# Performance work log

Hardware: AMD Instinct MI355X
Metric: run time of the kernel (lower is better)

## Reference

```python
import jax, jax.numpy as jnp
import numpy as np

C = 256

def setup_inputs() -> dict:
    key = jax.random.key(0)
    ks = jax.random.split(key, 7)
    s = 1.0 / np.sqrt(C)
    x = jax.random.normal(ks[0], (4, C, 64, 64), dtype=jnp.float32)
    Wq = jax.random.uniform(ks[1], (C, C), jnp.float32, -s, s)
    bq = jax.random.uniform(ks[2], (C,), jnp.float32, -s, s)
    Wk = jax.random.uniform(ks[3], (C, C), jnp.float32, -s, s)
    bk = jax.random.uniform(ks[4], (C,), jnp.float32, -s, s)
    Wv = jax.random.uniform(ks[5], (C, C), jnp.float32, -s, s)
    bv = jax.random.uniform(ks[6], (C,), jnp.float32, -s, s)
    return {"x": x, "Wq": Wq, "bq": bq, "Wk": Wk, "bk": bk, "Wv": Wv, "bv": bv}

def reference(x, Wq, bq, Wk, bk, Wv, bv):
    B, Cc, H, W = x.shape
    N = H * W
    xf = x.reshape(B, Cc, N)                      # (B, C, N)
    # 1x1 conv == channel linear: out[b,o,n] = sum_c W[o,c] x[b,c,n] + b[o]
    q = jnp.einsum('oc,bcn->bno', Wq, xf) + bq    # (B, N, C)  proj_query^T
    k = jnp.einsum('oc,bcn->bon', Wk, xf) + bk[None, :, None]  # (B, C, N)
    v = jnp.einsum('oc,bcn->bon', Wv, xf) + bv[None, :, None]  # (B, C, N)
    energy = jnp.einsum('bnc,bcm->bnm', q, k)     # (B, N, N)
    attention = jax.nn.softmax(energy, axis=-1)
    # out = V @ attention^T : out[b,c,n] = sum_m v[b,c,m] * attention[b,n,m]
    out = jnp.einsum('bcm,bnm->bcn', v, attention)
    return out.reshape(B, Cc, H, W)
```

## Files before the change

kernel.cpp:

```cpp
#include <hip/hip_runtime.h>
#include <math.h>

#define BB 4
#define CC 256
#define NN 4096

using half8 = __attribute__((ext_vector_type(8))) _Float16;
using f32x4 = __attribute__((ext_vector_type(4))) float;

__device__ __forceinline__ unsigned short f2h(float f) {
  _Float16 h = (_Float16)f;
  return __builtin_bit_cast(unsigned short, h);
}

#define ASYNC16(g, l)                                                        \
  __builtin_amdgcn_global_load_lds(                                          \
      (const __attribute__((address_space(1))) unsigned int*)(g),            \
      (__attribute__((address_space(3))) unsigned int*)(l), 16, 0, 0)

__device__ __forceinline__ int kt_off(int r, int chunk) {
  return r * 256 + (((chunk & 24) | ((chunk ^ r) & 7)) << 3);
}
__device__ __forceinline__ int vt_off(int r, int chunk) {
  return r * 64 + (((chunk ^ r) & 7) << 3);
}

__global__ __launch_bounds__(256) void k_transpose(const float* __restrict__ x,
                                                   unsigned short* __restrict__ Xt) {
  __shared__ float tile[64][65];
  int b = blockIdx.z, c0 = blockIdx.y * 64, n0 = blockIdx.x * 64;
  int t = threadIdx.x;
  const float* xp = x + ((size_t)b * CC + c0) * NN + n0;
#pragma unroll
  for (int p = 0; p < 4; ++p) {
    int c = p * 16 + (t >> 4);
    int j = (t & 15) * 4;
    float4 v = *(const float4*)(xp + (size_t)c * NN + j);
    tile[c][j] = v.x; tile[c][j + 1] = v.y; tile[c][j + 2] = v.z; tile[c][j + 3] = v.w;
  }
  __syncthreads();
  unsigned short* xtp = Xt + ((size_t)b * NN + n0) * CC + c0;
#pragma unroll
  for (int p = 0; p < 2; ++p) {
    int n = p * 32 + (t >> 3);
    int cb = (t & 7) * 8;
    union { unsigned short u[8]; uint4 v; } tmp;
#pragma unroll
    for (int i = 0; i < 8; ++i) tmp.u[i] = f2h(tile[cb + i][n]);
    *(uint4*)(xtp + (size_t)n * CC + cb) = tmp.v;
  }
}

__global__ __launch_bounds__(256, 1) void k_proj(const unsigned short* __restrict__ Xt,
    const float* __restrict__ Wq, const float* __restrict__ bq,
    const float* __restrict__ Wk, const float* __restrict__ bk,
    const float* __restrict__ Wv, const float* __restrict__ bv,
    unsigned short* __restrict__ Q, unsigned short* __restrict__ K,
    unsigned short* __restrict__ V) {
  __shared__ union {
    struct { unsigned short xa[128][72]; unsigned short wb[256][72]; } s;
    unsigned short qo[128][264];
    unsigned short vo[256][136];
  } u;
  int proj = blockIdx.z;
  const float* W    = proj == 0 ? Wq : (proj == 1 ? Wk : Wv);
  const float* bias = proj == 0 ? bq : (proj == 1 ? bk : bv);
  int b = blockIdx.y, n0 = blockIdx.x * 128;
  int t = threadIdx.x, w = t >> 6, lane = t & 63, l15 = lane & 15, quad = lane >> 4;

  f32x4 z = {0.f, 0.f, 0.f, 0.f};
  f32x4 acc[2][16];
#pragma unroll
  for (int i = 0; i < 2; ++i)
#pragma unroll
    for (int j = 0; j < 16; ++j) acc[i][j] = z;

  for (int ks = 0; ks < 4; ++ks) {
    __syncthreads();
#pragma unroll
    for (int p = 0; p < 4; ++p) {
      int r = p * 32 + (t >> 3);
      *(uint4*)&u.s.xa[r][(t & 7) * 8] =
        *(const uint4*)(Xt + ((size_t)b * NN + n0 + r) * CC + ks * 64 + (t & 7) * 8);
    }
#pragma unroll
    for (int p = 0; p < 16; ++p) {
      int r = p * 16 + (t >> 4);
      float4 wv = *(const float4*)(W + (size_t)r * CC + ks * 64 + (t & 15) * 4);
      ushort4 pk;
      pk.x = f2h(wv.x); pk.y = f2h(wv.y); pk.z = f2h(wv.z); pk.w = f2h(wv.w);
      *(ushort4*)&u.s.wb[r][(t & 15) * 4] = pk;
    }
    __syncthreads();
#pragma unroll
    for (int kc = 0; kc < 2; ++kc) {
      half8 af[2];
#pragma unroll
      for (int nt = 0; nt < 2; ++nt)
        af[nt] = *(const half8*)&u.s.xa[w * 32 + nt * 16 + l15][kc * 32 + quad * 8];
#pragma unroll
      for (int ct = 0; ct < 16; ++ct) {
        half8 bf = *(const half8*)&u.s.wb[ct * 16 + l15][kc * 32 + quad * 8];
        acc[0][ct] = __builtin_amdgcn_mfma_f32_16x16x32_f16(af[0], bf, acc[0][ct], 0, 0, 0);
        acc[1][ct] = __builtin_amdgcn_mfma_f32_16x16x32_f16(af[1], bf, acc[1][ct], 0, 0, 0);
      }
    }
  }
#pragma unroll
  for (int ct = 0; ct < 16; ++ct) {
    float bv_ = bias[ct * 16 + l15];
#pragma unroll
    for (int nt = 0; nt < 2; ++nt)
#pragma unroll
      for (int r = 0; r < 4; ++r) acc[nt][ct][r] += bv_;
  }
  __syncthreads();
  if (proj < 2) {
#pragma unroll
    for (int nt = 0; nt < 2; ++nt)
#pragma unroll
      for (int ct = 0; ct < 16; ++ct)
#pragma unroll
        for (int r = 0; r < 4; ++r)
          u.qo[w * 32 + nt * 16 + quad * 4 + r][ct * 16 + l15] = f2h(acc[nt][ct][r]);
    __syncthreads();
    unsigned short* out = (proj == 0 ? Q : K) + ((size_t)b * NN + n0) * CC;
#pragma unroll
    for (int p = 0; p < 16; ++p) {
      int f = p * 4096 + t * 16;
      int n = f >> 9, ob = f & 511;
      *(uint4*)((char*)out + (size_t)n * 512 + ob) =
        *(const uint4*)((const char*)&u.qo[n][0] + ob);
    }
  } else {
#pragma unroll
    for (int nt = 0; nt < 2; ++nt)
#pragma unroll
      for (int ct = 0; ct < 16; ++ct)
#pragma unroll
        for (int r = 0; r < 4; ++r)
          u.vo[ct * 16 + l15][w * 32 + nt * 16 + quad * 4 + r] = f2h(acc[nt][ct][r]);
    __syncthreads();
    unsigned short* out = V + (size_t)b * CC * NN + n0;
#pragma unroll
    for (int p = 0; p < 16; ++p) {
      int o = p * 16 + (t >> 4);
      *(uint4*)((char*)out + (size_t)o * NN * 2 + (t & 15) * 16) =
        *(const uint4*)&u.vo[o][(t & 15) * 8];
    }
  }
}

__global__ __launch_bounds__(512) void k_flash(const unsigned short* __restrict__ Q,
    const unsigned short* __restrict__ K, const unsigned short* __restrict__ V,
    float* __restrict__ out, float* __restrict__ opart, float* __restrict__ ml,
    int n_splits) {
  __shared__ unsigned short ktA[16384], ktB[16384];
  __shared__ unsigned short vtA[16384], vtB[16384];
  __shared__ unsigned short pt[8192];
  int b = blockIdx.y, q0 = blockIdx.x * 128, split = blockIdx.z;
  int nper = 64 / n_splits;
  int t = threadIdx.x, w = t >> 6, lane = t & 63, l15 = lane & 15, quad = lane >> 4;

  half8 qf[8];
  const unsigned short* qrow = Q + ((size_t)b * NN + q0 + w * 16 + l15) * CC;
#pragma unroll
  for (int k = 0; k < 8; ++k) qf[k] = *(const half8*)(qrow + k * 32 + quad * 8);

  f32x4 z = {0.f, 0.f, 0.f, 0.f};
  f32x4 o_acc[16];
#pragma unroll
  for (int i = 0; i < 16; ++i) o_acc[i] = z;
  float m_i[4], lp_[4];
#pragma unroll
  for (int r = 0; r < 4; ++r) { m_i[r] = -INFINITY; lp_[r] = 0.f; }

  int it_beg = split * nper, it_end = it_beg + nper;

  auto dma_k = [&](int it, unsigned short* dst) {
    const char* kb = (const char*)(K + ((size_t)b * NN + it * 64) * CC);
#pragma unroll
    for (int p = 0; p < 4; ++p) {
      int c = p * 512 + t;
      int r = c >> 5, lo = c & 31;
      int chunk = (lo & 24) | ((lo ^ r) & 7);
      ASYNC16(kb + r * 512 + chunk * 16, &dst[(p * 512 + (w << 6)) * 8]);
    }
  };
  auto dma_v = [&](int it, unsigned short* dst) {
    const char* vb = (const char*)(V + (size_t)b * CC * NN + it * 64);
#pragma unroll
    for (int p = 0; p < 4; ++p) {
      int c = p * 512 + t;
      int r = c >> 3;
      int chunk = (c ^ r) & 7;
      ASYNC16(vb + (size_t)r * 8192 + chunk * 16, &dst[(p * 512 + (w << 6)) * 8]);
    }
  };

  auto body = [&](const unsigned short* ktc, const unsigned short* vtc,
                  unsigned short* ktn, unsigned short* vtn, int it) {
    if (it + 1 < it_end) { dma_k(it + 1, ktn); dma_v(it + 1, vtn); }

    f32x4 sa[4];
#pragma unroll
    for (int j = 0; j < 4; ++j) sa[j] = z;
#pragma unroll
    for (int k = 0; k < 8; ++k) {
#pragma unroll
      for (int j = 0; j < 4; ++j) {
        half8 bf = *(const half8*)&ktc[kt_off(j * 16 + l15, 4 * k + quad)];
        sa[j] = __builtin_amdgcn_mfma_f32_16x16x32_f16(qf[k], bf, sa[j], 0, 0, 0);
      }
    }
    float mt[4];
#pragma unroll
    for (int r = 0; r < 4; ++r)
      mt[r] = fmaxf(fmaxf(sa[0][r], sa[1][r]), fmaxf(sa[2][r], sa[3][r]));
#pragma unroll
    for (int off = 1; off < 16; off <<= 1)
#pragma unroll
      for (int r = 0; r < 4; ++r)
        mt[r] = fmaxf(mt[r], __shfl_xor(mt[r], off, 64));
    float alpha[4];
#pragma unroll
    for (int r = 0; r < 4; ++r) {
      float mn = fmaxf(m_i[r], mt[r]);
      alpha[r] = __expf(m_i[r] - mn);
      m_i[r] = mn;
    }
#pragma unroll
    for (int r = 0; r < 4; ++r) {
      float ls = 0.f;
#pragma unroll
      for (int j = 0; j < 4; ++j) {
        float p = __expf(sa[j][r] - m_i[r]);
        sa[j][r] = p;
        ls += p;
      }
      lp_[r] = lp_[r] * alpha[r] + ls;
    }
#pragma unroll
    for (int ct = 0; ct < 16; ++ct)
#pragma unroll
      for (int r = 0; r < 4; ++r) o_acc[ct][r] *= alpha[r];
#pragma unroll
    for (int j = 0; j < 4; ++j)
#pragma unroll
      for (int r = 0; r < 4; ++r) {
        int row = quad * 4 + r;
        int chunk = 2 * j + (l15 >> 3);
        pt[w * 1024 + row * 64 + (((chunk ^ row) & 7) << 3) + (l15 & 7)] = f2h(sa[j][r]);
      }
#pragma unroll
    for (int mc = 0; mc < 2; ++mc) {
      half8 af = *(const half8*)&pt[w * 1024 + l15 * 64 + ((((mc * 4 + quad) ^ l15) & 7) << 3)];
#pragma unroll
      for (int ct = 0; ct < 16; ++ct) {
        half8 bf = *(const half8*)&vtc[vt_off(ct * 16 + l15, mc * 4 + quad)];
        o_acc[ct] = __builtin_amdgcn_mfma_f32_16x16x32_f16(af, bf, o_acc[ct], 0, 0, 0);
      }
    }
    __syncthreads();
  };

  dma_k(it_beg, ktA);
  dma_v(it_beg, vtA);
  __syncthreads();

  for (int it = it_beg; it < it_end; it += 2) {
    body(ktA, vtA, ktB, vtB, it);
    body(ktB, vtB, ktA, vtA, it + 1);
  }

#pragma unroll
  for (int off = 1; off < 16; off <<= 1)
#pragma unroll
    for (int r = 0; r < 4; ++r)
      lp_[r] += __shfl_xor(lp_[r], off, 64);

  float sc[4];
#pragma unroll
  for (int r = 0; r < 4; ++r) sc[r] = (n_splits == 1) ? 1.f / lp_[r] : 1.f;

  float (*od)[128] = (float(*)[128])ktA;
  float* ob = (n_splits == 1 ? out : opart + (size_t)split * BB * CC * NN)
              + (size_t)b * CC * NN + q0;
#pragma unroll
  for (int qtr = 0; qtr < 4; ++qtr) {
    __syncthreads();
#pragma unroll
    for (int ct2 = 0; ct2 < 4; ++ct2) {
      int ct = qtr * 4 + ct2;
#pragma unroll
      for (int r = 0; r < 4; ++r)
        od[ct2 * 16 + l15][w * 16 + quad * 4 + r] = o_acc[ct][r] * sc[r];
    }
    __syncthreads();
#pragma unroll
    for (int pp = 0; pp < 4; ++pp) {
      int row = pp * 16 + (t >> 5);
      *(float4*)(ob + (size_t)(qtr * 64 + row) * NN + (t & 31) * 4) =
        *(const float4*)&od[row][(t & 31) * 4];
    }
  }
  if (n_splits != 1 && l15 == 0) {
    float* mp = ml + ((size_t)(split * 2 + 0) * BB + b) * NN + q0 + w * 16 + quad * 4;
    float* lq = ml + ((size_t)(split * 2 + 1) * BB + b) * NN + q0 + w * 16 + quad * 4;
#pragma unroll
    for (int r = 0; r < 4; ++r) { mp[r] = m_i[r]; lq[r] = lp_[r]; }
  }
}

__global__ __launch_bounds__(256) void k_merge(const float* __restrict__ opart,
    const float* __restrict__ ml, float* __restrict__ out) {
  size_t i = ((size_t)blockIdx.x * 256 + threadIdx.x) * 4;
  int n = (int)(i & (NN - 1));
  int b = (int)(i >> 20);
  float4 m1 = *(const float4*)(ml + (size_t)(0 * BB + b) * NN + n);
  float4 l1 = *(const float4*)(ml + (size_t)(1 * BB + b) * NN + n);
  float4 m2 = *(const float4*)(ml + (size_t)(2 * BB + b) * NN + n);
  float4 l2 = *(const float4*)(ml + (size_t)(3 * BB + b) * NN + n);
  float4 o1 = *(const float4*)(opart + i);
  float4 o2 = *(const float4*)(opart + (size_t)BB * CC * NN + i);
  float4 o;
#define MERGE1(f) { \
    float mm = fmaxf(m1.f, m2.f); \
    float e1 = __expf(m1.f - mm), e2 = __expf(m2.f - mm); \
    o.f = (e1 * o1.f + e2 * o2.f) / (e1 * l1.f + e2 * l2.f); }
  MERGE1(x) MERGE1(y) MERGE1(z) MERGE1(w)
#undef MERGE1
  *(float4*)(out + i) = o;
}

extern "C" void kernel_launch(void* const* d_in, const int* in_sizes, int n_in,
                              void* d_out, int out_size, void* d_ws, size_t ws_size,
                              hipStream_t stream) {
  const float* x  = (const float*)d_in[0];
  const float* Wq = (const float*)d_in[1];
  const float* bq = (const float*)d_in[2];
  const float* Wk = (const float*)d_in[3];
  const float* bk = (const float*)d_in[4];
  const float* Wv = (const float*)d_in[5];
  const float* bv = (const float*)d_in[6];
  float* out = (float*)d_out;
  char* ws = (char*)d_ws;
  unsigned short* Xt = (unsigned short*)(ws);
  unsigned short* Qb = (unsigned short*)(ws + (size_t)8  * 1024 * 1024);
  unsigned short* Kb = (unsigned short*)(ws + (size_t)16 * 1024 * 1024);
  unsigned short* Vb = (unsigned short*)(ws + (size_t)24 * 1024 * 1024);
  float* Opart = (float*)(ws + (size_t)32 * 1024 * 1024);
  float* Ml    = (float*)(ws + (size_t)64 * 1024 * 1024);

  k_transpose<<<dim3(64, 4, 4), 256, 0, stream>>>(x, Xt);
  k_proj<<<dim3(32, 4, 3), 256, 0, stream>>>(Xt, Wq, bq, Wk, bk, Wv, bv, Qb, Kb, Vb);

  bool split2 = ws_size >= (size_t)68 * 1024 * 1024;
  if (split2) {
    k_flash<<<dim3(32, 4, 2), 512, 0, stream>>>(Qb, Kb, Vb, out, Opart, Ml, 2);
    k_merge<<<dim3(4096), 256, 0, stream>>>(Opart, Ml, out);
  } else {
    k_flash<<<dim3(32, 4, 1), 512, 0, stream>>>(Qb, Kb, Vb, out, Opart, Ml, 1);
  }
}
```

Measured before the change: 219.3 us.

## Halve flash workgroup to 4 waves with two query tiles each, reuse K/V fragments

The flash kernel now runs 4 waves of 256 threads instead of 8, and each wave handles 32 query rows as two 16-row M-tiles. Every K and V fragment read from LDS therefore feeds two MFMAs, halving LDS traffic per MFMA. Q is staged in LDS instead of registers, and the K/V double buffers become single buffers: V's load is issued at the start of each iteration and the next K tile is prefetched after the QK^T phase. The cost is twice the accumulator registers per wave (launch_bounds 256,1), fewer waves to hide latency, and less overlap of loads with compute.

```diff
diff --git a/kernel.cpp b/kernel.cpp
--- a/kernel.cpp
+++ b/kernel.cpp
@@ -18,7 +18,7 @@
       (const __attribute__((address_space(1))) unsigned int*)(g),            \
       (__attribute__((address_space(3))) unsigned int*)(l), 16, 0, 0)
 
-__device__ __forceinline__ int kt_off(int r, int chunk) {
+__device__ __forceinline__ int row512_off(int r, int chunk) {
   return r * 256 + (((chunk & 24) | ((chunk ^ r) & 7)) << 3);
 }
 __device__ __forceinline__ int vt_off(int r, int chunk) {
@@ -151,164 +151,198 @@
   }
 }
 
-__global__ __launch_bounds__(512) void k_flash(const unsigned short* __restrict__ Q,
+__global__ __launch_bounds__(256, 1) void k_flash(const unsigned short* __restrict__ Q,
     const unsigned short* __restrict__ K, const unsigned short* __restrict__ V,
     float* __restrict__ out, float* __restrict__ opart, float* __restrict__ ml,
     int n_splits) {
-  __shared__ unsigned short ktA[16384], ktB[16384];
-  __shared__ unsigned short vtA[16384], vtB[16384];
+  __shared__ unsigned short qa[32768];
+  __shared__ unsigned short kt[16384];
+  __shared__ unsigned short vt[16384];
   __shared__ unsigned short pt[8192];
   int b = blockIdx.y, q0 = blockIdx.x * 128, split = blockIdx.z;
   int nper = 64 / n_splits;
   int t = threadIdx.x, w = t >> 6, lane = t & 63, l15 = lane & 15, quad = lane >> 4;
 
-  half8 qf[8];
-  const unsigned short* qrow = Q + ((size_t)b * NN + q0 + w * 16 + l15) * CC;
-#pragma unroll
-  for (int k = 0; k < 8; ++k) qf[k] = *(const half8*)(qrow + k * 32 + quad * 8);
-
   f32x4 z = {0.f, 0.f, 0.f, 0.f};
-  f32x4 o_acc[16];
-#pragma unroll
-  for (int i = 0; i < 16; ++i) o_acc[i] = z;
-  float m_i[4], lp_[4];
-#pragma unroll
-  for (int r = 0; r < 4; ++r) { m_i[r] = -INFINITY; lp_[r] = 0.f; }
+  f32x4 o_acc[2][16];
+#pragma unroll
+  for (int mt = 0; mt < 2; ++mt)
+#pragma unroll
+    for (int i = 0; i < 16; ++i) o_acc[mt][i] = z;
+  float m_i[2][4], lp_[2][4];
+#pragma unroll
+  for (int mt = 0; mt < 2; ++mt)
+#pragma unroll
+    for (int r = 0; r < 4; ++r) { m_i[mt][r] = -INFINITY; lp_[mt][r] = 0.f; }
 
   int it_beg = split * nper, it_end = it_beg + nper;
 
-  auto dma_k = [&](int it, unsigned short* dst) {
+  auto dma_k = [&](int it) {
     const char* kb = (const char*)(K + ((size_t)b * NN + it * 64) * CC);
 #pragma unroll
-    for (int p = 0; p < 4; ++p) {
-      int c = p * 512 + t;
+    for (int p = 0; p < 8; ++p) {
+      int c = p * 256 + t;
       int r = c >> 5, lo = c & 31;
       int chunk = (lo & 24) | ((lo ^ r) & 7);
-      ASYNC16(kb + r * 512 + chunk * 16, &dst[(p * 512 + (w << 6)) * 8]);
+      ASYNC16(kb + r * 512 + chunk * 16, &kt[(p * 256 + (w << 6)) * 8]);
     }
   };
-  auto dma_v = [&](int it, unsigned short* dst) {
+  auto dma_v = [&](int it) {
     const char* vb = (const char*)(V + (size_t)b * CC * NN + it * 64);
 #pragma unroll
-    for (int p = 0; p < 4; ++p) {
-      int c = p * 512 + t;
+    for (int p = 0; p < 8; ++p) {
+      int c = p * 256 + t;
       int r = c >> 3;
       int chunk = (c ^ r) & 7;
-      ASYNC16(vb + (size_t)r * 8192 + chunk * 16, &dst[(p * 512 + (w << 6)) * 8]);
+      ASYNC16(vb + (size_t)r * 8192 + chunk * 16, &vt[(p * 256 + (w << 6)) * 8]);
     }
   };
 
-  auto body = [&](const unsigned short* ktc, const unsigned short* vtc,
-                  unsigned short* ktn, unsigned short* vtn, int it) {
-    if (it + 1 < it_end) { dma_k(it + 1, ktn); dma_v(it + 1, vtn); }
-
-    f32x4 sa[4];
-#pragma unroll
-    for (int j = 0; j < 4; ++j) sa[j] = z;
-#pragma unroll
-    for (int k = 0; k < 8; ++k) {
+  {
+    const char* qb = (const char*)(Q + ((size_t)b * NN + q0) * CC);
+#pragma unroll
+    for (int p = 0; p < 16; ++p) {
+      int c = p * 256 + t;
+      int r = c >> 5, lo = c & 31;
+      int chunk = (lo & 24) | ((lo ^ r) & 7);
+      ASYNC16(qb + r * 512 + chunk * 16, &qa[(p * 256 + (w << 6)) * 8]);
+    }
+    dma_k(it_beg);
+  }
+  __syncthreads();
+
+  for (int it = it_beg; it < it_end; ++it) {
+    dma_v(it);
+
+    f32x4 sa[2][4];
+#pragma unroll
+    for (int mt = 0; mt < 2; ++mt)
+#pragma unroll
+      for (int j = 0; j < 4; ++j) sa[mt][j] = z;
+#pragma unroll
+    for (int kk = 0; kk < 8; ++kk) {
+      half8 af[2];
+#pragma unroll
+      for (int mt = 0; mt < 2; ++mt)
+        af[mt] = *(const half8*)&qa[row512_off(w * 32 + mt * 16 + l15, kk * 4 + quad)];
 #pragma unroll
       for (int j = 0; j < 4; ++j) {
-        half8 bf = *(const half8*)&ktc[kt_off(j * 16 + l15, 4 * k + quad)];
-        sa[j] = __builtin_amdgcn_mfma_f32_16x16x32_f16(qf[k], bf, sa[j], 0, 0, 0);
-      }
-    }
-    float mt[4];
+        half8 bf = *(const half8*)&kt[row512_off(j * 16 + l15, kk * 4 + quad)];
+#pragma unroll
+        for (int mt = 0; mt < 2; ++mt)
+          sa[mt][j] = __builtin_amdgcn_mfma_f32_16x16x32_f16(af[mt], bf, sa[mt][j], 0, 0, 0);
+      }
+    }
+    __syncthreads();
+    if (it + 1 < it_end) dma_k(it + 1);
+
+#pragma unroll
+    for (int mt = 0; mt < 2; ++mt) {
+      float mtx[4];
+#pragma unroll
+      for (int r = 0; r < 4; ++r)
+        mtx[r] = fmaxf(fmaxf(sa[mt][0][r], sa[mt][1][r]), fmaxf(sa[mt][2][r], sa[mt][3][r]));
+#pragma unroll
+      for (int off = 1; off < 16; off <<= 1)
+#pragma unroll
+        for (int r = 0; r < 4; ++r)
+          mtx[r] = fmaxf(mtx[r], __shfl_xor(mtx[r], off, 64));
+      float alpha[4];
+#pragma unroll
+      for (int r = 0; r < 4; ++r) {
+        float mn = fmaxf(m_i[mt][r], mtx[r]);
+        alpha[r] = __expf(m_i[mt][r] - mn);
+        m_i[mt][r] = mn;
+      }
+#pragma unroll
+      for (int r = 0; r < 4; ++r) {
+        float ls = 0.f;
+#pragma unroll
+        for (int j = 0; j < 4; ++j) {
+          float p = __expf(sa[mt][j][r] - m_i[mt][r]);
+          sa[mt][j][r] = p;
+          ls += p;
+        }
+        lp_[mt][r] = lp_[mt][r] * alpha[r] + ls;
+      }
+#pragma unroll
+      for (int ct = 0; ct < 16; ++ct)
+#pragma unroll
+        for (int r = 0; r < 4; ++r) o_acc[mt][ct][r] *= alpha[r];
+#pragma unroll
+      for (int j = 0; j < 4; ++j)
+#pragma unroll
+        for (int r = 0; r < 4; ++r) {
+          int row = mt * 16 + quad * 4 + r;
+          int chunk = 2 * j + (l15 >> 3);
+          pt[w * 2048 + row * 64 + (((chunk ^ row) & 7) << 3) + (l15 & 7)] = f2h(sa[mt][j][r]);
+        }
+    }
+#pragma unroll
+    for (int kk2 = 0; kk2 < 2; ++kk2) {
+      half8 af[2];
+#pragma unroll
+      for (int mt = 0; mt < 2; ++mt) {
+        int row = mt * 16 + l15;
+        af[mt] = *(const half8*)&pt[w * 2048 + row * 64 + ((((kk2 * 4 + quad) ^ row) & 7) << 3)];
+      }
+#pragma unroll
+      for (int ct = 0; ct < 16; ++ct) {
+        half8 bf = *(const half8*)&vt[vt_off(ct * 16 + l15, kk2 * 4 + quad)];
+#pragma unroll
+        for (int mt = 0; mt < 2; ++mt)
+          o_acc[mt][ct] = __builtin_amdgcn_mfma_f32_16x16x32_f16(af[mt], bf, o_acc[mt][ct], 0, 0, 0);
+      }
+    }
+    __syncthreads();
+  }
+
+#pragma unroll
+  for (int off = 1; off < 16; off <<= 1)
+#pragma unroll
+    for (int mt = 0; mt < 2; ++mt)
+#pragma unroll
+      for (int r = 0; r < 4; ++r)
+        lp_[mt][r] += __shfl_xor(lp_[mt][r], off, 64);
+
+  float sc[2][4];
+#pragma unroll
+  for (int mt = 0; mt < 2; ++mt)
 #pragma unroll
     for (int r = 0; r < 4; ++r)
-      mt[r] = fmaxf(fmaxf(sa[0][r], sa[1][r]), fmaxf(sa[2][r], sa[3][r]));
-#pragma unroll
-    for (int off = 1; off < 16; off <<= 1)
-#pragma unroll
-      for (int r = 0; r < 4; ++r)
-        mt[r] = fmaxf(mt[r], __shfl_xor(mt[r], off, 64));
-    float alpha[4];
-#pragma unroll
-    for (int r = 0; r < 4; ++r) {
-      float mn = fmaxf(m_i[r], mt[r]);
-      alpha[r] = __expf(m_i[r] - mn);
-      m_i[r] = mn;
-    }
-#pragma unroll
-    for (int r = 0; r < 4; ++r) {
-      float ls = 0.f;
-#pragma unroll
-      for (int j = 0; j < 4; ++j) {
-        float p = __expf(sa[j][r] - m_i[r]);
-        sa[j][r] = p;
-        ls += p;
-      }
-      lp_[r] = lp_[r] * alpha[r] + ls;
-    }
-#pragma unroll
-    for (int ct = 0; ct < 16; ++ct)
-#pragma unroll
-      for (int r = 0; r < 4; ++r) o_acc[ct][r] *= alpha[r];
-#pragma unroll
-    for (int j = 0; j < 4; ++j)
-#pragma unroll
-      for (int r = 0; r < 4; ++r) {
-        int row = quad * 4 + r;
-        int chunk = 2 * j + (l15 >> 3);
-        pt[w * 1024 + row * 64 + (((chunk ^ row) & 7) << 3) + (l15 & 7)] = f2h(sa[j][r]);
-      }
-#pragma unroll
-    for (int mc = 0; mc < 2; ++mc) {
-      half8 af = *(const half8*)&pt[w * 1024 + l15 * 64 + ((((mc * 4 + quad) ^ l15) & 7) << 3)];
-#pragma unroll
-      for (int ct = 0; ct < 16; ++ct) {
-        half8 bf = *(const half8*)&vtc[vt_off(ct * 16 + l15, mc * 4 + quad)];
-        o_acc[ct] = __builtin_amdgcn_mfma_f32_16x16x32_f16(af, bf, o_acc[ct], 0, 0, 0);
-      }
-    }
-    __syncthreads();
-  };
-
-  dma_k(it_beg, ktA);
-  dma_v(it_beg, vtA);
-  __syncthreads();
-
-  for (int it = it_beg; it < it_end; it += 2) {
-    body(ktA, vtA, ktB, vtB, it);
-    body(ktB, vtB, ktA, vtA, it + 1);
-  }
-
-#pragma unroll
-  for (int off = 1; off < 16; off <<= 1)
-#pragma unroll
-    for (int r = 0; r < 4; ++r)
-      lp_[r] += __shfl_xor(lp_[r], off, 64);
-
-  float sc[4];
-#pragma unroll
-  for (int r = 0; r < 4; ++r) sc[r] = (n_splits == 1) ? 1.f / lp_[r] : 1.f;
-
-  float (*od)[128] = (float(*)[128])ktA;
+      sc[mt][r] = (n_splits == 1) ? 1.f / lp_[mt][r] : 1.f;
+
+  float* od = (float*)qa;
   float* ob = (n_splits == 1 ? out : opart + (size_t)split * BB * CC * NN)
               + (size_t)b * CC * NN + q0;
 #pragma unroll
-  for (int qtr = 0; qtr < 4; ++qtr) {
-    __syncthreads();
-#pragma unroll
-    for (int ct2 = 0; ct2 < 4; ++ct2) {
-      int ct = qtr * 4 + ct2;
-#pragma unroll
-      for (int r = 0; r < 4; ++r)
-        od[ct2 * 16 + l15][w * 16 + quad * 4 + r] = o_acc[ct][r] * sc[r];
-    }
-    __syncthreads();
-#pragma unroll
-    for (int pp = 0; pp < 4; ++pp) {
-      int row = pp * 16 + (t >> 5);
-      *(float4*)(ob + (size_t)(qtr * 64 + row) * NN + (t & 31) * 4) =
-        *(const float4*)&od[row][(t & 31) * 4];
+  for (int pp = 0; pp < 8; ++pp) {
+    __syncthreads();
+#pragma unroll
+    for (int cp = 0; cp < 2; ++cp) {
+      int ct = pp * 2 + cp;
+#pragma unroll
+      for (int mt = 0; mt < 2; ++mt)
+#pragma unroll
+        for (int r = 0; r < 4; ++r)
+          od[(cp * 16 + l15) * 132 + w * 32 + mt * 16 + quad * 4 + r] =
+              o_acc[mt][ct][r] * sc[mt][r];
+    }
+    __syncthreads();
+#pragma unroll
+    for (int p2 = 0; p2 < 4; ++p2) {
+      int row = p2 * 8 + (t >> 5);
+      *(float4*)(ob + (size_t)(pp * 32 + row) * NN + (t & 31) * 4) =
+        *(const float4*)&od[row * 132 + (t & 31) * 4];
     }
   }
   if (n_splits != 1 && l15 == 0) {
-    float* mp = ml + ((size_t)(split * 2 + 0) * BB + b) * NN + q0 + w * 16 + quad * 4;
-    float* lq = ml + ((size_t)(split * 2 + 1) * BB + b) * NN + q0 + w * 16 + quad * 4;
-#pragma unroll
-    for (int r = 0; r < 4; ++r) { mp[r] = m_i[r]; lq[r] = lp_[r]; }
+    float* mp = ml + ((size_t)(split * 2 + 0) * BB + b) * NN + q0 + w * 32 + quad * 4;
+    float* lq = ml + ((size_t)(split * 2 + 1) * BB + b) * NN + q0 + w * 32 + quad * 4;
+#pragma unroll
+    for (int mt = 0; mt < 2; ++mt)
+#pragma unroll
+      for (int r = 0; r < 4; ++r) { mp[mt * 16 + r] = m_i[mt][r]; lq[mt * 16 + r] = lp_[mt][r]; }
   }
 }
 
@@ -357,9 +391,9 @@
 
   bool split2 = ws_size >= (size_t)68 * 1024 * 1024;
   if (split2) {
-    k_flash<<<dim3(32, 4, 2), 512, 0, stream>>>(Qb, Kb, Vb, out, Opart, Ml, 2);
+    k_flash<<<dim3(32, 4, 2), 256, 0, stream>>>(Qb, Kb, Vb, out, Opart, Ml, 2);
     k_merge<<<dim3(4096), 256, 0, stream>>>(Opart, Ml, out);
   } else {
-    k_flash<<<dim3(32, 4, 1), 512, 0, stream>>>(Qb, Kb, Vb, out, Opart, Ml, 1);
-  }
-}
+    k_flash<<<dim3(32, 4, 1), 256, 0, stream>>>(Qb, Kb, Vb, out, Opart, Ml, 1);
+  }
+}
```

New measurement: 260.0 us. +18.6%, slower.
